# Kernel optimization log

Measured on AMD Instinct MI355X. Metric: run time of the kernel, lower is better.

## Reference

```python
import jax, jax.numpy as jnp
import numpy as np
import math

B, H, L, D = 2, 16, 2048, 128
NEG = float(-2**32 + 1)  # module uses -2**32+1 instead of -inf to avoid softmax NaN on fully-masked rows


def setup_inputs() -> dict:
    key = jax.random.key(0)
    kq, kk, kv, km, kp = jax.random.split(key, 5)
    return {
        "Q": jax.random.normal(kq, (B, H, L, D), dtype=jnp.float32),
        "K": jax.random.normal(kk, (B, H, L, D), dtype=jnp.float32),
        "V": jax.random.normal(kv, (B, H, L, D), dtype=jnp.float32),
        "attn_mask": jax.random.normal(km, (L, L), dtype=jnp.float32),  # additive bias mask
        "padding_mask": jax.random.randint(kp, (B, L), 0, 2).astype(bool),  # True -> masked
    }


def reference(Q, K, V, attn_mask, padding_mask):
    scale = math.sqrt(Q.shape[-1])
    # energy: [B, H, Lq, Lk]
    energy = jnp.einsum("bhqd,bhkd->bhqk", Q, K) / scale
    energy = energy + attn_mask[None, None, :, :]
    energy = jnp.where(padding_mask[:, None, None, :], NEG, energy)
    attention_weight = jax.nn.softmax(energy, axis=-1)
    # dropout=None in eval semantics -> identity
    x = jnp.einsum("bhqk,bhkd->bhqd", attention_weight, V)
    return (x, attention_weight)
```

## Files before the change

kernel.cpp:

```cpp
#include <hip/hip_runtime.h>


typedef __attribute__((ext_vector_type(8))) __bf16 bf16x8;
typedef __attribute__((ext_vector_type(4))) float f32x4;

#define L_SEQ 2048
#define D_H   128
#define R_Q   128
#define C_K   64
#define NTHR  512
#define KPITCH 136
#define VPITCH 72
#define NKT   (L_SEQ / C_K)

__device__ __forceinline__ unsigned short f2bf(float f) {
    unsigned int u = __float_as_uint(f);
    unsigned int r = (u + 0x7FFFu + ((u >> 16) & 1u)) >> 16;
    return (unsigned short)r;
}

__device__ __forceinline__ float fexp2(float x) {
#if __has_builtin(__builtin_amdgcn_exp2f)
    return __builtin_amdgcn_exp2f(x);
#else
    return exp2f(x);
#endif
}

__device__ __forceinline__ float rsum16(float v) {
#pragma unroll
    for (int o = 1; o < 16; o <<= 1) v += __shfl_xor(v, o, 64);
    return v;
}

__device__ __forceinline__ void block_sync() {
    __builtin_amdgcn_sched_barrier(0);
    asm volatile("s_waitcnt lgkmcnt(0)");
    __builtin_amdgcn_s_barrier();
    __builtin_amdgcn_sched_barrier(0);
}

union BF8 {
    bf16x8 v;
    unsigned short s[8];
    uint4 u;
};

__global__ __launch_bounds__(NTHR, 4) void attn_kernel(
    const float* __restrict__ Q, const float* __restrict__ K,
    const float* __restrict__ V, const float* __restrict__ mask,
    const int* __restrict__ pad, float* __restrict__ Xout,
    float* __restrict__ Pout)
{
    __shared__ unsigned short Ks[C_K * KPITCH];
    __shared__ unsigned short Vt[D_H * VPITCH];
    __shared__ unsigned short Ps[R_Q * VPITCH];
    __shared__ float PadB[L_SEQ];

    const int tid  = threadIdx.x;
    const int wave = tid >> 6;
    const int lane = tid & 63;
    const int quad = lane >> 4;
    const int l16  = lane & 15;

    const int bh = blockIdx.x & 31;
    const int qt = blockIdx.x >> 5;
    const int b  = bh >> 4;

    const float LOG2E  = 1.44269504088896340736f;
    const float SCALE2 = 0.08838834764831845f * 1.44269504088896340736f;

    const float* Kg0 = K + (long long)bh * L_SEQ * D_H;
    const float* Vg0 = V + (long long)bh * L_SEQ * D_H;

    BF8 qf[4];
    {
        const float4* qrow = reinterpret_cast<const float4*>(
            Q + ((long long)bh * L_SEQ + qt * R_Q + wave * 16 + l16) * D_H);
#pragma unroll
        for (int kb = 0; kb < 4; ++kb) {
            float4 a = qrow[kb * 8 + quad * 2];
            float4 c = qrow[kb * 8 + quad * 2 + 1];
            qf[kb].s[0] = f2bf(a.x); qf[kb].s[1] = f2bf(a.y);
            qf[kb].s[2] = f2bf(a.z); qf[kb].s[3] = f2bf(a.w);
            qf[kb].s[4] = f2bf(c.x); qf[kb].s[5] = f2bf(c.y);
            qf[kb].s[6] = f2bf(c.z); qf[kb].s[7] = f2bf(c.w);
        }
    }
#pragma unroll
    for (int i = 0; i < 4; ++i) {
        int idx = tid + i * NTHR;
        PadB[idx] = pad[b * L_SEQ + idx] ? -INFINITY : 0.0f;
    }

    float4 kpre[4];
    float  vpre[16];

    auto issueK = [&](int kt) {
        const float4* Kg = reinterpret_cast<const float4*>(Kg0 + (long long)kt * C_K * D_H);
#pragma unroll
        for (int i = 0; i < 2; ++i) {
            int c = tid + i * NTHR;
            kpre[2 * i]     = Kg[c * 2];
            kpre[2 * i + 1] = Kg[c * 2 + 1];
        }
    };
    auto writeK = [&]() {
#pragma unroll
        for (int i = 0; i < 2; ++i) {
            int c = tid + i * NTHR;
            int row = c >> 4, off = (c & 15) * 8;
            float4 a = kpre[2 * i];
            float4 d = kpre[2 * i + 1];
            BF8 t;
            t.s[0] = f2bf(a.x); t.s[1] = f2bf(a.y); t.s[2] = f2bf(a.z); t.s[3] = f2bf(a.w);
            t.s[4] = f2bf(d.x); t.s[5] = f2bf(d.y); t.s[6] = f2bf(d.z); t.s[7] = f2bf(d.w);
            *reinterpret_cast<uint4*>(&Ks[row * KPITCH + off]) = t.u;
        }
    };
    auto issueV = [&](int kt) {
        const float* Vg = Vg0 + (long long)kt * C_K * D_H;
        int c = tid & 127;
#pragma unroll
        for (int i = 0; i < 2; ++i) {
            int key0 = (((tid >> 7) + i * 4) << 3);
#pragma unroll
            for (int j = 0; j < 8; ++j)
                vpre[i * 8 + j] = Vg[(key0 + j) * D_H + c];
        }
    };
    auto writeV = [&]() {
        int c = tid & 127;
#pragma unroll
        for (int i = 0; i < 2; ++i) {
            int key0 = (((tid >> 7) + i * 4) << 3);
            BF8 t;
#pragma unroll
            for (int j = 0; j < 8; ++j) t.s[j] = f2bf(vpre[i * 8 + j]);
            *reinterpret_cast<uint4*>(&Vt[c * VPITCH + key0]) = t.u;
        }
    };

    auto computeS = [&](f32x4* sacc) {
        f32x4 z4 = {0.f, 0.f, 0.f, 0.f};
#pragma unroll
        for (int ct = 0; ct < 4; ++ct) sacc[ct] = z4;
#pragma unroll
        for (int kb = 0; kb < 4; ++kb) {
#pragma unroll
            for (int ct = 0; ct < 4; ++ct) {
                bf16x8 bk = *reinterpret_cast<const bf16x8*>(
                    &Ks[(ct * 16 + l16) * KPITCH + kb * 32 + quad * 8]);
                sacc[ct] = __builtin_amdgcn_mfma_f32_16x16x32_bf16(qf[kb].v, bk, sacc[ct], 0, 0, 0);
            }
        }
    };

    const long long qrow0 = (long long)(qt * R_Q + wave * 16 + quad * 4);
    const float* maskBase = mask + qrow0 * L_SEQ;

    float lpart[4] = {0.f, 0.f, 0.f, 0.f};
    issueK(0);
    writeK();
    for (int kt = 0; kt < NKT; ++kt) {
        block_sync();
        if (kt + 1 < NKT) issueK(kt + 1);
        float mk[4][4], pb[4];
#pragma unroll
        for (int ct = 0; ct < 4; ++ct) {
            int kc = kt * C_K + ct * 16 + l16;
            pb[ct] = PadB[kc];
#pragma unroll
            for (int r = 0; r < 4; ++r) mk[ct][r] = maskBase[(long long)r * L_SEQ + kc];
        }
        f32x4 sacc[4];
        computeS(sacc);
#pragma unroll
        for (int ct = 0; ct < 4; ++ct)
#pragma unroll
            for (int r = 0; r < 4; ++r) {
                float m2 = fmaf(mk[ct][r], LOG2E, pb[ct]);
                float e2 = fmaf(sacc[ct][r], SCALE2, m2);
                lpart[r] += fexp2(e2);
            }
        block_sync();
        if (kt + 1 < NKT) writeK();
    }

    float rinv[4];
#pragma unroll
    for (int r = 0; r < 4; ++r) {
        float l = rsum16(lpart[r]);
        rinv[r] = (l > 0.f) ? (1.0f / l) : 0.f;
    }

    f32x4 oacc[8];
    {
        f32x4 z4 = {0.f, 0.f, 0.f, 0.f};
#pragma unroll
        for (int ct = 0; ct < 8; ++ct) oacc[ct] = z4;
    }
    float* PoutBase = Pout + ((long long)bh * L_SEQ + (qt * R_Q + quad * 4 + wave * 16)) * L_SEQ;

    issueK(0);
    issueV(0);
    writeK();
    writeV();
    for (int kt = 0; kt < NKT; ++kt) {
        block_sync();
        if (kt + 1 < NKT) { issueK(kt + 1); issueV(kt + 1); }
        float mk[4][4], pb[4];
#pragma unroll
        for (int ct = 0; ct < 4; ++ct) {
            int kc = kt * C_K + ct * 16 + l16;
            pb[ct] = PadB[kc];
#pragma unroll
            for (int r = 0; r < 4; ++r) mk[ct][r] = maskBase[(long long)r * L_SEQ + kc];
        }
        f32x4 sacc[4];
        computeS(sacc);
#pragma unroll
        for (int ct = 0; ct < 4; ++ct) {
            int kc = kt * C_K + ct * 16 + l16;
#pragma unroll
            for (int r = 0; r < 4; ++r) {
                float m2 = fmaf(mk[ct][r], LOG2E, pb[ct]);
                float e2 = fmaf(sacc[ct][r], SCALE2, m2);
                float p  = fexp2(e2) * rinv[r];
                __builtin_nontemporal_store(p, &PoutBase[(long long)r * L_SEQ + kc]);
                Ps[(wave * 16 + quad * 4 + r) * VPITCH + ct * 16 + l16] = f2bf(p);
            }
        }
#pragma unroll
        for (int kd = 0; kd < 2; ++kd) {
            bf16x8 ap = *reinterpret_cast<const bf16x8*>(
                &Ps[(wave * 16 + l16) * VPITCH + kd * 32 + quad * 8]);
#pragma unroll
            for (int ct = 0; ct < 8; ++ct) {
                bf16x8 bv = *reinterpret_cast<const bf16x8*>(
                    &Vt[(ct * 16 + l16) * VPITCH + kd * 32 + quad * 8]);
                oacc[ct] = __builtin_amdgcn_mfma_f32_16x16x32_bf16(ap, bv, oacc[ct], 0, 0, 0);
            }
        }
        block_sync();
        if (kt + 1 < NKT) { writeK(); writeV(); }
    }

    float* Xg = Xout + ((long long)bh * L_SEQ + qt * R_Q + wave * 16 + quad * 4) * D_H;
#pragma unroll
    for (int ct = 0; ct < 8; ++ct)
#pragma unroll
        for (int r = 0; r < 4; ++r)
            __builtin_nontemporal_store(oacc[ct][r], &Xg[r * D_H + ct * 16 + l16]);
}

extern "C" void kernel_launch(void* const* d_in, const int* in_sizes, int n_in,
                              void* d_out, int out_size, void* d_ws, size_t ws_size,
                              hipStream_t stream) {
    const float* Q    = (const float*)d_in[0];
    const float* K    = (const float*)d_in[1];
    const float* V    = (const float*)d_in[2];
    const float* mask = (const float*)d_in[3];
    const int*   pad  = (const int*)d_in[4];
    float* Xout = (float*)d_out;
    float* Pout = (float*)d_out + (long long)2 * 16 * 2048 * 128;
    attn_kernel<<<dim3(512), dim3(NTHR), 0, stream>>>(Q, K, V, mask, pad, Xout, Pout);
}
```

Measured before the change: 888.3 us.

## Pre-convert K/V to bf16 in a prep kernel and stream pass-1 K from registers

Adds a prep kernel that converts K to bf16 and V to transposed bf16 tiles in workspace, so the attention kernel loads half the bytes and skips per-block conversion and the strided V transpose. The first (row-sum) pass now reads K fragments straight from global into registers with double buffering, dropping LDS staging and barriers. A fallback kernel is kept for when the workspace is too small. This costs an extra launch and a workspace round trip, and the pass-1 global fragment loads may be less coalesced.

```diff
diff --git a/kernel.cpp b/kernel.cpp
--- a/kernel.cpp
+++ b/kernel.cpp
@@ -12,6 +12,7 @@
 #define KPITCH 136
 #define VPITCH 72
 #define NKT   (L_SEQ / C_K)
+#define NBH   32
 
 __device__ __forceinline__ unsigned short f2bf(float f) {
     unsigned int u = __float_as_uint(f);
@@ -46,7 +47,254 @@
     uint4 u;
 };
 
+__global__ __launch_bounds__(256) void prep_kernel(
+    const float* __restrict__ K, const float* __restrict__ V,
+    unsigned short* __restrict__ Kbf, unsigned short* __restrict__ Vbf)
+{
+    __shared__ float Vld[C_K][D_H + 4];
+    const int blk = blockIdx.x;
+    const int bh  = blk >> 5, kt = blk & 31;
+    const int tid = threadIdx.x;
+
+    const float* Kt = K + ((size_t)bh * L_SEQ + (size_t)kt * C_K) * D_H;
+    const float* Vt = V + ((size_t)bh * L_SEQ + (size_t)kt * C_K) * D_H;
+    unsigned short* Ko = Kbf + ((size_t)bh * NKT + kt) * (C_K * D_H);
+    unsigned short* Vo = Vbf + ((size_t)bh * NKT + kt) * (C_K * D_H);
+
+#pragma unroll
+    for (int i = 0; i < 4; ++i) {
+        int c = tid + i * 256;
+        const float4* s = reinterpret_cast<const float4*>(Kt) + c * 2;
+        float4 a = s[0], b = s[1];
+        BF8 t;
+        t.s[0] = f2bf(a.x); t.s[1] = f2bf(a.y); t.s[2] = f2bf(a.z); t.s[3] = f2bf(a.w);
+        t.s[4] = f2bf(b.x); t.s[5] = f2bf(b.y); t.s[6] = f2bf(b.z); t.s[7] = f2bf(b.w);
+        *reinterpret_cast<uint4*>(&Ko[c * 8]) = t.u;
+    }
+#pragma unroll
+    for (int i = 0; i < 8; ++i) {
+        int fc = tid + i * 256;
+        int row = fc >> 5, c4 = fc & 31;
+        *reinterpret_cast<float4*>(&Vld[row][c4 * 4]) = reinterpret_cast<const float4*>(Vt)[fc];
+    }
+    __syncthreads();
+#pragma unroll
+    for (int i = 0; i < 4; ++i) {
+        int ch = tid + i * 256;
+        int d = ch >> 3, key0 = (ch & 7) * 8;
+        BF8 t;
+#pragma unroll
+        for (int j = 0; j < 8; ++j) t.s[j] = f2bf(Vld[key0 + j][d]);
+        *reinterpret_cast<uint4*>(&Vo[ch * 8]) = t.u;
+    }
+}
+
 __global__ __launch_bounds__(NTHR, 4) void attn_kernel(
+    const float* __restrict__ Q, const unsigned short* __restrict__ Kbf,
+    const unsigned short* __restrict__ Vbf, const float* __restrict__ mask,
+    const int* __restrict__ pad, float* __restrict__ Xout,
+    float* __restrict__ Pout)
+{
+    __shared__ unsigned short Ks[C_K * KPITCH];
+    __shared__ unsigned short Vt[D_H * VPITCH];
+    __shared__ unsigned short Ps[R_Q * VPITCH];
+    __shared__ float PadB[L_SEQ];
+
+    const int tid  = threadIdx.x;
+    const int wave = tid >> 6;
+    const int lane = tid & 63;
+    const int quad = lane >> 4;
+    const int l16  = lane & 15;
+
+    const int bh = blockIdx.x & 31;
+    const int qt = blockIdx.x >> 5;
+    const int b  = bh >> 4;
+
+    const float LOG2E  = 1.44269504088896340736f;
+    const float SCALE2 = 0.08838834764831845f * 1.44269504088896340736f;
+
+    const unsigned short* Kbh = Kbf + (size_t)bh * NKT * (C_K * D_H);
+    const unsigned short* Vbh = Vbf + (size_t)bh * NKT * (C_K * D_H);
+
+    BF8 qf[4];
+    {
+        const float4* qrow = reinterpret_cast<const float4*>(
+            Q + ((size_t)bh * L_SEQ + qt * R_Q + wave * 16 + l16) * D_H);
+#pragma unroll
+        for (int kb = 0; kb < 4; ++kb) {
+            float4 a = qrow[kb * 8 + quad * 2];
+            float4 c = qrow[kb * 8 + quad * 2 + 1];
+            qf[kb].s[0] = f2bf(a.x); qf[kb].s[1] = f2bf(a.y);
+            qf[kb].s[2] = f2bf(a.z); qf[kb].s[3] = f2bf(a.w);
+            qf[kb].s[4] = f2bf(c.x); qf[kb].s[5] = f2bf(c.y);
+            qf[kb].s[6] = f2bf(c.z); qf[kb].s[7] = f2bf(c.w);
+        }
+    }
+#pragma unroll
+    for (int i = 0; i < 4; ++i) {
+        int idx = tid + i * NTHR;
+        PadB[idx] = pad[b * L_SEQ + idx] ? -INFINITY : 0.0f;
+    }
+    __syncthreads();
+
+    const long long qrow0 = (long long)(qt * R_Q + wave * 16 + quad * 4);
+    const float* maskBase = mask + qrow0 * L_SEQ;
+
+    float lpart[4] = {0.f, 0.f, 0.f, 0.f};
+    {
+        BF8 fr[2][4];
+        auto issueFrag = [&](int slot, int kt, int kb) {
+            const unsigned short* Ktile = Kbh + (size_t)kt * (C_K * D_H);
+#pragma unroll
+            for (int ct = 0; ct < 4; ++ct)
+                fr[slot][ct].u = *reinterpret_cast<const uint4*>(
+                    &Ktile[(ct * 16 + l16) * D_H + kb * 32 + quad * 8]);
+        };
+        issueFrag(0, 0, 0);
+        issueFrag(1, 0, 1);
+        for (int kt = 0; kt < NKT; ++kt) {
+            float mk[4][4], pb[4];
+#pragma unroll
+            for (int ct = 0; ct < 4; ++ct) {
+                int kc = kt * C_K + ct * 16 + l16;
+                pb[ct] = PadB[kc];
+#pragma unroll
+                for (int r = 0; r < 4; ++r) mk[ct][r] = maskBase[(long long)r * L_SEQ + kc];
+            }
+            f32x4 sacc[4];
+            f32x4 z4 = {0.f, 0.f, 0.f, 0.f};
+#pragma unroll
+            for (int ct = 0; ct < 4; ++ct) sacc[ct] = z4;
+#pragma unroll
+            for (int kb = 0; kb < 4; ++kb) {
+                const int slot = kb & 1;
+#pragma unroll
+                for (int ct = 0; ct < 4; ++ct)
+                    sacc[ct] = __builtin_amdgcn_mfma_f32_16x16x32_bf16(
+                        qf[kb].v, fr[slot][ct].v, sacc[ct], 0, 0, 0);
+                int nkb = kb + 2, nkt = kt;
+                if (nkb >= 4) { nkb -= 4; ++nkt; }
+                if (nkt < NKT) issueFrag(slot, nkt, nkb);
+            }
+#pragma unroll
+            for (int ct = 0; ct < 4; ++ct)
+#pragma unroll
+                for (int r = 0; r < 4; ++r) {
+                    float m2 = fmaf(mk[ct][r], LOG2E, pb[ct]);
+                    float e2 = fmaf(sacc[ct][r], SCALE2, m2);
+                    lpart[r] += fexp2(e2);
+                }
+        }
+    }
+
+    float rinv[4];
+#pragma unroll
+    for (int r = 0; r < 4; ++r) {
+        float l = rsum16(lpart[r]);
+        rinv[r] = (l > 0.f) ? (1.0f / l) : 0.f;
+    }
+
+    f32x4 oacc[8];
+    {
+        f32x4 z4 = {0.f, 0.f, 0.f, 0.f};
+#pragma unroll
+        for (int ct = 0; ct < 8; ++ct) oacc[ct] = z4;
+    }
+    float* PoutBase = Pout + ((size_t)bh * L_SEQ + (qt * R_Q + wave * 16 + quad * 4)) * L_SEQ;
+
+    uint4 kpre2[2], vpre2[2];
+    auto issueK2 = [&](int kt) {
+        const uint4* Kt4 = reinterpret_cast<const uint4*>(Kbh + (size_t)kt * (C_K * D_H));
+        kpre2[0] = Kt4[tid];
+        kpre2[1] = Kt4[tid + NTHR];
+    };
+    auto writeK2 = [&]() {
+#pragma unroll
+        for (int i = 0; i < 2; ++i) {
+            int c = tid + i * NTHR;
+            *reinterpret_cast<uint4*>(&Ks[(c >> 4) * KPITCH + (c & 15) * 8]) = kpre2[i];
+        }
+    };
+    auto issueV2 = [&](int kt) {
+        const uint4* Vt4 = reinterpret_cast<const uint4*>(Vbh + (size_t)kt * (C_K * D_H));
+        vpre2[0] = Vt4[tid];
+        vpre2[1] = Vt4[tid + NTHR];
+    };
+    auto writeV2 = [&]() {
+#pragma unroll
+        for (int i = 0; i < 2; ++i) {
+            int ch = tid + i * NTHR;
+            *reinterpret_cast<uint4*>(&Vt[(ch >> 3) * VPITCH + (ch & 7) * 8]) = vpre2[i];
+        }
+    };
+
+    issueK2(0);
+    issueV2(0);
+    writeK2();
+    writeV2();
+    for (int kt = 0; kt < NKT; ++kt) {
+        block_sync();
+        if (kt + 1 < NKT) { issueK2(kt + 1); issueV2(kt + 1); }
+        float mk[4][4], pb[4];
+#pragma unroll
+        for (int ct = 0; ct < 4; ++ct) {
+            int kc = kt * C_K + ct * 16 + l16;
+            pb[ct] = PadB[kc];
+#pragma unroll
+            for (int r = 0; r < 4; ++r) mk[ct][r] = maskBase[(long long)r * L_SEQ + kc];
+        }
+        f32x4 sacc[4];
+        {
+            f32x4 z4 = {0.f, 0.f, 0.f, 0.f};
+#pragma unroll
+            for (int ct = 0; ct < 4; ++ct) sacc[ct] = z4;
+#pragma unroll
+            for (int kb = 0; kb < 4; ++kb) {
+#pragma unroll
+                for (int ct = 0; ct < 4; ++ct) {
+                    bf16x8 bk = *reinterpret_cast<const bf16x8*>(
+                        &Ks[(ct * 16 + l16) * KPITCH + kb * 32 + quad * 8]);
+                    sacc[ct] = __builtin_amdgcn_mfma_f32_16x16x32_bf16(
+                        qf[kb].v, bk, sacc[ct], 0, 0, 0);
+                }
+            }
+        }
+#pragma unroll
+        for (int ct = 0; ct < 4; ++ct) {
+            int kc = kt * C_K + ct * 16 + l16;
+#pragma unroll
+            for (int r = 0; r < 4; ++r) {
+                float m2 = fmaf(mk[ct][r], LOG2E, pb[ct]);
+                float e2 = fmaf(sacc[ct][r], SCALE2, m2);
+                float p  = fexp2(e2) * rinv[r];
+                __builtin_nontemporal_store(p, &PoutBase[(long long)r * L_SEQ + kc]);
+                Ps[(wave * 16 + quad * 4 + r) * VPITCH + ct * 16 + l16] = f2bf(p);
+            }
+        }
+#pragma unroll
+        for (int kd = 0; kd < 2; ++kd) {
+            bf16x8 ap = *reinterpret_cast<const bf16x8*>(
+                &Ps[(wave * 16 + l16) * VPITCH + kd * 32 + quad * 8]);
+#pragma unroll
+            for (int ct = 0; ct < 8; ++ct) {
+                bf16x8 bv = *reinterpret_cast<const bf16x8*>(
+                    &Vt[(ct * 16 + l16) * VPITCH + kd * 32 + quad * 8]);
+                oacc[ct] = __builtin_amdgcn_mfma_f32_16x16x32_bf16(ap, bv, oacc[ct], 0, 0, 0);
+            }
+        }
+        block_sync();
+        if (kt + 1 < NKT) { writeK2(); writeV2(); }
+    }
+
+    float* Xg = Xout + ((size_t)bh * L_SEQ + qt * R_Q + wave * 16 + quad * 4) * D_H;
+#pragma unroll
+    for (int ct = 0; ct < 8; ++ct)
+#pragma unroll
+        for (int r = 0; r < 4; ++r)
+            __builtin_nontemporal_store(oacc[ct][r], &Xg[r * D_H + ct * 16 + l16]);
+}
+
+__global__ __launch_bounds__(NTHR, 4) void attn_kernel_fb(
     const float* __restrict__ Q, const float* __restrict__ K,
     const float* __restrict__ V, const float* __restrict__ mask,
     const int* __restrict__ pad, float* __restrict__ Xout,
@@ -264,5 +512,16 @@
     const int*   pad  = (const int*)d_in[4];
     float* Xout = (float*)d_out;
     float* Pout = (float*)d_out + (long long)2 * 16 * 2048 * 128;
-    attn_kernel<<<dim3(512), dim3(NTHR), 0, stream>>>(Q, K, V, mask, pad, Xout, Pout);
-}
+
+    const size_t kv_elems = (size_t)NBH * L_SEQ * D_H;
+    const size_t need     = 2 * kv_elems * sizeof(unsigned short);
+
+    if (d_ws != nullptr && ws_size >= need) {
+        unsigned short* Kbf = (unsigned short*)d_ws;
+        unsigned short* Vbf = Kbf + kv_elems;
+        prep_kernel<<<dim3(NBH * NKT), dim3(256), 0, stream>>>(K, V, Kbf, Vbf);
+        attn_kernel<<<dim3(512), dim3(NTHR), 0, stream>>>(Q, Kbf, Vbf, mask, pad, Xout, Pout);
+    } else {
+        attn_kernel_fb<<<dim3(512), dim3(NTHR), 0, stream>>>(Q, K, V, mask, pad, Xout, Pout);
+    }
+}
```

New measurement: 1.071 ms. 20.5% more time.
